# Kernel tuning notes

Measured on AMD Instinct MI355X. Metric: run time of the kernel, lower is better.

## Reference

```python
import jax, jax.numpy as jnp
import numpy as np

INPUT_SIZE = 784
HIDDEN = 512
NUM_CLASSES = 10
BATCH = 65536


def _linear_params(key, fan_in, fan_out):
    # torch nn.Linear default init: U(-1/sqrt(fan_in), 1/sqrt(fan_in))
    kw, kb = jax.random.split(key)
    bound = 1.0 / np.sqrt(fan_in)
    W = jax.random.uniform(kw, (fan_in, fan_out), jnp.float32, -bound, bound)
    b = jax.random.uniform(kb, (fan_out,), jnp.float32, -bound, bound)
    return W, b


def setup_inputs() -> dict:
    key = jax.random.key(0)
    keys = jax.random.split(key, 9)
    inp = {"x": jax.random.normal(keys[0], (BATCH, INPUT_SIZE), jnp.float32)}
    dims = [(INPUT_SIZE, HIDDEN)] + [(HIDDEN, HIDDEN)] * 6 + [(HIDDEN, NUM_CLASSES)]
    for i, (fi, fo) in enumerate(dims):
        W, b = _linear_params(keys[i + 1], fi, fo)
        inp[f"W{i + 1}"] = W
        inp[f"b{i + 1}"] = b
    return inp


def _dropout(x, p, key):
    # torch F.dropout (training=True): inverted dropout, keep prob = 1-p
    keep = jax.random.bernoulli(key, 1.0 - p, x.shape)
    return jnp.where(keep, x / (1.0 - p), 0.0).astype(x.dtype)


def reference(x, W1, b1, W2, b2, W3, b3, W4, b4, W5, b5, W6, b6, W7, b7, W8, b8):
    dk = jax.random.split(jax.random.key(42), 3)
    h = jax.nn.relu(x @ W1 + b1)                       # h1 + relu
    h = jax.nn.relu(_dropout(h @ W2 + b2, 0.2, dk[0])) # h2 + dropout(0.2) + relu
    h = jax.nn.relu(h @ W3 + b3)                       # h3 + relu
    h = jax.nn.relu(_dropout(h @ W4 + b4, 0.3, dk[1])) # h4 + dropout(0.3) + relu
    h = jax.nn.relu(h @ W5 + b5)                       # h5 + relu
    h = jax.nn.relu(_dropout(h @ W6 + b6, 0.5, dk[2])) # h6 + dropout(0.5) + relu
    h = jax.nn.relu(h @ W7 + b7)                       # h7 + relu
    logits = h @ W8 + b8                               # h8
    return jax.nn.softmax(logits, axis=-1)
```

## Files before the change

kernel.cpp:

```cpp
#include <hip/hip_runtime.h>
#include <cstdint>

#define ROTL32(v,n) (((v) << (n)) | ((v) >> (32 - (n))))

__host__ __forceinline__ void tf2x32(uint32_t k0, uint32_t k1,
                                     uint32_t x0, uint32_t x1,
                                     uint32_t& o0, uint32_t& o1)
{
  uint32_t k2 = k0 ^ k1 ^ 0x1BD11BDAu;
  x0 += k0; x1 += k1;
#define TF_RND(r) { x0 += x1; x1 = ROTL32(x1, (r)); x1 ^= x0; }
  TF_RND(13) TF_RND(15) TF_RND(26) TF_RND(6)
  x0 += k1; x1 += k2 + 1u;
  TF_RND(17) TF_RND(29) TF_RND(16) TF_RND(24)
  x0 += k2; x1 += k0 + 2u;
  TF_RND(13) TF_RND(15) TF_RND(26) TF_RND(6)
  x0 += k0; x1 += k1 + 3u;
  TF_RND(17) TF_RND(29) TF_RND(16) TF_RND(24)
  x0 += k1; x1 += k2 + 4u;
  TF_RND(13) TF_RND(15) TF_RND(26) TF_RND(6)
  x0 += k2; x1 += k0 + 5u;
#undef TF_RND
  o0 = x0; o1 = x1;
}

__device__ __forceinline__ void tf2x32_d(uint32_t k0, uint32_t k1,
                                         uint32_t x0, uint32_t x1,
                                         uint32_t& o0, uint32_t& o1)
{
  uint32_t k2 = k0 ^ k1 ^ 0x1BD11BDAu;
  x0 += k0; x1 += k1;
#define R_(r) { x0 += x1; x1 = __builtin_rotateleft32(x1, (r)); x1 ^= x0; }
  R_(13) R_(15) R_(26) R_(6)
  x0 += k1; x1 += k2 + 1u;
  R_(17) R_(29) R_(16) R_(24)
  x0 += k2; x1 += k0 + 2u;
  R_(13) R_(15) R_(26) R_(6)
  x0 += k0; x1 += k1 + 3u;
  R_(17) R_(29) R_(16) R_(24)
  x0 += k1; x1 += k2 + 4u;
  R_(13) R_(15) R_(26) R_(6)
  x0 += k2; x1 += k0 + 5u;
#undef R_
  o0 = x0; o1 = x1;
}

typedef __attribute__((ext_vector_type(8))) _Float16 h16x8;
typedef __attribute__((ext_vector_type(4))) float fl32x4;
typedef __attribute__((ext_vector_type(2))) unsigned long long u64x2;

__device__ __forceinline__ float u2unit_f(uint32_t b) {
  uint32_t r = (b >> 9) | 0x3F800000u;
  float f; __builtin_memcpy(&f, &r, 4); return f - 1.0f;
}

#define GLD16(gp, lp) \
  __builtin_amdgcn_global_load_lds( \
      (__attribute__((address_space(1))) void*)(gp), \
      (__attribute__((address_space(3))) void*)(lp), 16, 0, 0)

#define VMW(n) asm volatile("s_waitcnt vmcnt(" #n ")" ::: "memory")
#define LKW0() asm volatile("s_waitcnt lgkmcnt(0)" ::: "memory")
#define SBAR() asm volatile("s_barrier" ::: "memory")

__global__ __launch_bounds__(256) void cvt_x_f(const float* __restrict__ x,
                                               _Float16* __restrict__ xp,
                                               unsigned long long* __restrict__ m0,
                                               uint32_t k0, uint32_t k1)
{
  int idx = blockIdx.x * 256 + threadIdx.x;
  int row = idx / 104, c = idx - row * 104;
  h16x8 o = {0,0,0,0,0,0,0,0};
  if (c < 98) {
    const fl32x4* p = (const fl32x4*)&x[row * 784 + c * 8];
    fl32x4 a = p[0], b = p[1];
    o[0] = (_Float16)a[0]; o[1] = (_Float16)a[1]; o[2] = (_Float16)a[2]; o[3] = (_Float16)a[3];
    o[4] = (_Float16)b[0]; o[5] = (_Float16)b[1]; o[6] = (_Float16)b[2]; o[7] = (_Float16)b[3];
  }
  *(h16x8*)&xp[row * 832 + c * 8] = o;

  uint32_t lane = threadIdx.x & 63u;
  uint32_t gw = (uint32_t)blockIdx.x * 4u + ((uint32_t)threadIdx.x >> 6);
#pragma unroll
  for (int i = 0; i < 3; ++i) {
    uint32_t wix = gw * 3u + (uint32_t)i;
    uint32_t b1, b2;
    tf2x32_d(k0, k1, 0u, wix * 64u + lane, b1, b2);
    unsigned long long mw = __ballot(u2unit_f(b1 ^ b2) < 0.8f);
    if (lane == 0) m0[wix] = mw;
  }
}

__global__ __launch_bounds__(256) void cvt_w_f(
    const float* __restrict__ W1, const float* __restrict__ W2, const float* __restrict__ W3,
    const float* __restrict__ W4, const float* __restrict__ W5, const float* __restrict__ W6,
    const float* __restrict__ W7, _Float16* __restrict__ WT1, _Float16* __restrict__ WT,
    unsigned long long* __restrict__ m0, uint32_t k0, uint32_t k1)
{
  int b = blockIdx.x;
  if (b < 1666) {
    int idx = b * 256 + threadIdx.x;
    int n = idx / 832, k = idx - n * 832;
    WT1[idx] = (k < 784) ? (_Float16)W1[k * 512 + n] : (_Float16)0.f;
  } else {
    int l = (b - 1666) >> 10;
    int idx = ((b - 1666) & 1023) * 256 + threadIdx.x;
    int n = idx >> 9, k = idx & 511;
    const float* Wp = (l == 0) ? W2 : (l == 1) ? W3 : (l == 2) ? W4
                    : (l == 3) ? W5 : (l == 4) ? W6 : W7;
    WT[l * 262144 + idx] = (_Float16)Wp[k * 512 + n];
  }
  uint32_t lane = threadIdx.x & 63u;
  uint32_t gw = (uint32_t)blockIdx.x * 4u + ((uint32_t)threadIdx.x >> 6);
#pragma unroll
  for (int i = 0; i < 7; ++i) {
    uint32_t wix = 319488u + gw * 7u + (uint32_t)i;
    if (wix < 524288u) {
      uint32_t b1, b2;
      tf2x32_d(k0, k1, 0u, wix * 64u + lane, b1, b2);
      unsigned long long mw = __ballot(u2unit_f(b1 ^ b2) < 0.8f);
      if (lane == 0) m0[wix] = mw;
    }
  }
}

template<bool DROP>
__global__ __launch_bounds__(256, 4) void gemm_r(
    const _Float16* __restrict__ A, const _Float16* __restrict__ BT,
    const float* __restrict__ bias, const unsigned long long* __restrict__ mask,
    float invq, _Float16* __restrict__ C, int K,
    unsigned long long* __restrict__ mout, uint32_t mbase, int tfcap, int tfpp,
    uint32_t mk0, uint32_t mk1, float mq)
{
  __shared__ __align__(16) _Float16 sm[16384];
  const int tid  = threadIdx.x;
  const int lane = tid & 63;
  const int wv   = tid >> 6;
  const int wr   = wv >> 1, wc = wv & 1;
  const int rml  = lane & 15;
  const int kq   = lane >> 4;

  int bid = blockIdx.x;
  int t = (bid & 7) * 256 + (bid >> 3);
  int bm = (t >> 2) * 128;
  int bn = (t & 3) * 128;

  const _Float16* Ab = A + (size_t)bm * K;
  const _Float16* Bb = BT + (size_t)bn * K;

  const int sp   = tid >> 3;
  const int sin  = (tid & 7) ^ (sp & 7);
  const int srow = 2 * sp + (sin >> 2);
  const int sk16 = sin & 3;

  const int rslot = (((rml & 1) << 2) | kq) ^ (rml >> 1);
  const int abase = (wr * 32 + (rml >> 1)) * 64 + rslot * 8;
  const int bbase = 4096 + (wc * 32 + (rml >> 1)) * 64 + rslot * 8;

  fl32x4 acc[4][4];
#pragma unroll
  for (int i = 0; i < 4; ++i)
#pragma unroll
    for (int j = 0; j < 4; ++j)
      acc[i][j] = (fl32x4){0.f, 0.f, 0.f, 0.f};

  const int nst = K >> 5;

#define STAGE(selem, kt) do {                                                  \
    GLD16(Ab + (size_t)srow * K + (kt) * 32 + sk16 * 8,                        \
          sm + (selem) + wv * 512);                                            \
    GLD16(Ab + (size_t)(srow + 64) * K + (kt) * 32 + sk16 * 8,                 \
          sm + (selem) + 2048 + wv * 512);                                     \
    GLD16(Bb + (size_t)srow * K + (kt) * 32 + sk16 * 8,                        \
          sm + (selem) + 4096 + wv * 512);                                     \
    GLD16(Bb + (size_t)(srow + 64) * K + (kt) * 32 + sk16 * 8,                 \
          sm + (selem) + 6144 + wv * 512);                                     \
  } while (0)

  STAGE(0, 0);

  uint64_t mw0 = 0;
  int tfc = 0;
  uint32_t gw = (uint32_t)bid * 4u + (uint32_t)wv;

#pragma unroll 1
  for (int kt = 0; kt < nst; ++kt) {
    const int slot = (kt & 1) * 8192;
    if (kt + 1 < nst) STAGE(8192 - slot, kt + 1);
    if (mout != nullptr) {
      int todo = tfcap - tfc; if (todo > tfpp) todo = tfpp;
      for (int i_ = 0; i_ < todo; ++i_) {
        uint32_t a_, b_;
        tf2x32_d(mk0, mk1, 0u,
                 (mbase + gw * (uint32_t)tfcap + (uint32_t)tfc) * 64u + (uint32_t)lane,
                 a_, b_);
        unsigned long long bal = __ballot(u2unit_f(a_ ^ b_) < mq);
        if (lane == tfc) mw0 = bal;
        ++tfc;
      }
    }
    if (kt + 1 < nst) { VMW(4); } else { VMW(0); }
    SBAR();
    h16x8 af[4], bf[4];
#pragma unroll
    for (int mf = 0; mf < 4; ++mf)
      af[mf] = *(const h16x8*)&sm[slot + abase + mf * 512];
#pragma unroll
    for (int nf = 0; nf < 4; ++nf)
      bf[nf] = *(const h16x8*)&sm[slot + bbase + nf * 512];
#pragma unroll
    for (int mf = 0; mf < 4; ++mf)
#pragma unroll
      for (int nf = 0; nf < 4; ++nf)
        acc[mf][nf] = __builtin_amdgcn_mfma_f32_16x16x32_f16(af[mf], bf[nf], acc[mf][nf], 0, 0, 0);
    SBAR();
  }
#undef STAGE

  if (mout != nullptr && lane < tfcap)
    mout[mbase + gw * (uint32_t)tfcap + (uint32_t)lane] = mw0;

  const int eb = wv * 2176;
  const int lrr = lane >> 1;
  const int cbase = (lane & 1) * 4;

#define EPIHALF(HALF) do {                                                     \
    _Pragma("unroll")                                                          \
    for (int nf = 0; nf < 4; ++nf) {                                           \
      int colq = nf * 16 + rml;                                                \
      float bv = bias[bn + wc * 64 + colq];                                    \
      _Pragma("unroll")                                                        \
      for (int mfh = 0; mfh < 2; ++mfh) {                                      \
        _Pragma("unroll")                                                      \
        for (int r = 0; r < 4; ++r) {                                          \
          int lr = mfh * 16 + kq * 4 + r;                                      \
          float v = fmaxf(acc[(HALF) * 2 + mfh][nf][r] + bv, 0.0f) * invq;     \
          sm[eb + lr * 68 + colq] = (_Float16)v;                               \
        }                                                                      \
      }                                                                        \
    }                                                                          \
    LKW0();                                                                    \
    {                                                                          \
      int grow = bm + wr * 64 + (HALF) * 32 + lrr;                             \
      int col0 = bn + wc * 64;                                                 \
      uint64_t mw = 0;                                                         \
      if (DROP) mw = mask[(size_t)grow * 8 + (size_t)(col0 >> 6)];             \
      _Pragma("unroll")                                                        \
      for (int c = 0; c < 4; ++c) {                                            \
        int cc = cbase + c;                                                    \
        uint64_t lo = *(const uint64_t*)&sm[eb + lrr * 68 + cc * 8];           \
        uint64_t hi = *(const uint64_t*)&sm[eb + lrr * 68 + cc * 8 + 4];       \
        if (DROP) {                                                            \
          uint32_t bits = (uint32_t)(mw >> (cc * 8)) & 0xffu;                  \
          uint64_t klo = 0, khi = 0;                                           \
          if (bits & 0x01u) klo |= 0x000000000000ffffull;                      \
          if (bits & 0x02u) klo |= 0x00000000ffff0000ull;                      \
          if (bits & 0x04u) klo |= 0x0000ffff00000000ull;                      \
          if (bits & 0x08u) klo |= 0xffff000000000000ull;                      \
          if (bits & 0x10u) khi |= 0x000000000000ffffull;                      \
          if (bits & 0x20u) khi |= 0x00000000ffff0000ull;                      \
          if (bits & 0x40u) khi |= 0x0000ffff00000000ull;                      \
          if (bits & 0x80u) khi |= 0xffff000000000000ull;                      \
          lo &= klo; hi &= khi;                                                \
        }                                                                      \
        u64x2 ov; ov[0] = lo; ov[1] = hi;                                      \
        *(u64x2*)&C[(size_t)grow * 512 + col0 + cc * 8] = ov;                  \
      }                                                                        \
    }                                                                          \
  } while (0)

  EPIHALF(0);
  EPIHALF(1);
#undef EPIHALF
}

__global__ __launch_bounds__(256) void head_f(
    const _Float16* __restrict__ H, const float* __restrict__ W8,
    const float* __restrict__ b8, float* __restrict__ out)
{
  __shared__ float Wl[5120];
  for (int i = threadIdx.x; i < 5120; i += 256) Wl[i] = W8[i];
  __syncthreads();
  int lane = threadIdx.x & 63;
  int wv = threadIdx.x >> 6;
  int row = blockIdx.x * 4 + wv;
  h16x8 h = *(const h16x8*)&H[(size_t)row * 512 + lane * 8];
  float acc[10];
#pragma unroll
  for (int n = 0; n < 10; ++n) acc[n] = 0.f;
#pragma unroll
  for (int j = 0; j < 8; ++j) {
    float hf = (float)h[j];
    const float* wrow = &Wl[(lane * 8 + j) * 10];
#pragma unroll
    for (int n = 0; n < 10; ++n) acc[n] += hf * wrow[n];
  }
#pragma unroll
  for (int off = 1; off < 64; off <<= 1) {
#pragma unroll
    for (int n = 0; n < 10; ++n) acc[n] += __shfl_xor(acc[n], off);
  }
  if (lane == 0) {
    float mx = -3.0e38f;
#pragma unroll
    for (int n = 0; n < 10; ++n) { acc[n] += b8[n]; mx = fmaxf(mx, acc[n]); }
    float s = 0.f, e[10];
#pragma unroll
    for (int n = 0; n < 10; ++n) { e[n] = expf(acc[n] - mx); s += e[n]; }
    float is = 1.0f / s;
#pragma unroll
    for (int n = 0; n < 10; ++n) out[(size_t)row * 10 + n] = e[n] * is;
  }
}

extern "C" void kernel_launch(void* const* d_in, const int* in_sizes, int n_in,
                              void* d_out, int out_size, void* d_ws, size_t ws_size,
                              hipStream_t stream) {
  (void)in_sizes; (void)n_in; (void)out_size; (void)ws_size;
  const float* x = (const float*)d_in[0];
  const float* W[8]; const float* B[8];
  for (int i = 0; i < 8; ++i) { W[i] = (const float*)d_in[1 + 2*i]; B[i] = (const float*)d_in[2 + 2*i]; }

  char* w = (char*)d_ws;
  _Float16* xpad = (_Float16*)(w);
  _Float16* hA   = (_Float16*)(w + 109051904);
  _Float16* hB   = (_Float16*)(w + 176160768);
  _Float16* WT1  = (_Float16*)(w + 243269632);
  _Float16* WT   = (_Float16*)(w + 244121600);
  unsigned long long* masks = (unsigned long long*)(w + 247267328);
  unsigned long long* mL0 = masks;
  unsigned long long* mL1 = masks + 524288;
  unsigned long long* mL2 = masks + 1048576;

  uint32_t d00,d01,d10,d11,d20,d21;
  tf2x32(0u, 42u, 0u, 0u, d00, d01);
  tf2x32(0u, 42u, 0u, 1u, d10, d11);
  tf2x32(0u, 42u, 0u, 2u, d20, d21);

  cvt_x_f<<<26624, 256, 0, stream>>>(x, xpad, mL0, d00, d01);
  cvt_w_f<<<7810, 256, 0, stream>>>(W[0],W[1],W[2],W[3],W[4],W[5],W[6], WT1, WT,
                                    mL0, d00, d01);

  dim3 g(2048), b(256);
  gemm_r<false><<<g, b, 0, stream>>>(xpad, WT1,           B[0], nullptr, 1.0f,      hA, 832,
                                     nullptr, 0u, 0, 0, 0u, 0u, 0.f);
  gemm_r<true ><<<g, b, 0, stream>>>(hA,   WT + 0*262144, B[1], mL0,     1.0f/0.8f, hB, 512,
                                     mL1, 0u,       32, 2, d10, d11, 0.7f);
  gemm_r<false><<<g, b, 0, stream>>>(hB,   WT + 1*262144, B[2], nullptr, 1.0f,      hA, 512,
                                     mL1, 262144u,  32, 2, d10, d11, 0.7f);
  gemm_r<true ><<<g, b, 0, stream>>>(hA,   WT + 2*262144, B[3], mL1,     1.0f/0.7f, hB, 512,
                                     mL2, 0u,       32, 2, d20, d21, 0.5f);
  gemm_r<false><<<g, b, 0, stream>>>(hB,   WT + 3*262144, B[4], nullptr, 1.0f,      hA, 512,
                                     mL2, 262144u,  32, 2, d20, d21, 0.5f);
  gemm_r<true ><<<g, b, 0, stream>>>(hA,   WT + 4*262144, B[5], mL2,     2.0f,      hB, 512,
                                     nullptr, 0u, 0, 0, 0u, 0u, 0.f);
  gemm_r<false><<<g, b, 0, stream>>>(hB,   WT + 5*262144, B[6], nullptr, 1.0f,      hA, 512,
                                     nullptr, 0u, 0, 0, 0u, 0u, 0.f);
  head_f<<<16384, 256, 0, stream>>>(hA, W[7], B[7], (float*)d_out);
}
```

Baseline: 676.8 us.

## Fuse final linear head into last GEMM epilogue with partial logits

```diff
diff --git a/kernel.cpp b/kernel.cpp
--- a/kernel.cpp
+++ b/kernel.cpp
@@ -124,13 +124,14 @@
   }
 }
 
-template<bool DROP>
+template<bool DROP, bool HEAD>
 __global__ __launch_bounds__(256, 4) void gemm_r(
     const _Float16* __restrict__ A, const _Float16* __restrict__ BT,
     const float* __restrict__ bias, const unsigned long long* __restrict__ mask,
     float invq, _Float16* __restrict__ C, int K,
     unsigned long long* __restrict__ mout, uint32_t mbase, int tfcap, int tfpp,
-    uint32_t mk0, uint32_t mk1, float mq)
+    uint32_t mk0, uint32_t mk1, float mq,
+    const float* __restrict__ W8g, float* __restrict__ plog)
 {
   __shared__ __align__(16) _Float16 sm[16384];
   const int tid  = threadIdx.x;
@@ -219,6 +220,45 @@
 
   if (mout != nullptr && lane < tfcap)
     mout[mbase + gw * (uint32_t)tfcap + (uint32_t)lane] = mw0;
+
+  if (HEAD) {
+    __syncthreads();
+    float* W8l = (float*)sm;
+    for (int i = tid; i < 1280; i += 256) {
+      int k = i / 10, c = i - k * 10;
+      W8l[i] = W8g[(size_t)(bn + k) * 10 + c];
+    }
+    __syncthreads();
+    float* pout = plog + (size_t)((t & 3) * 2 + wc) * 655360;
+#pragma unroll
+    for (int mf = 0; mf < 4; ++mf) {
+#pragma unroll
+      for (int r = 0; r < 4; ++r) {
+        float p[10];
+#pragma unroll
+        for (int c = 0; c < 10; ++c) p[c] = 0.f;
+#pragma unroll
+        for (int nf = 0; nf < 4; ++nf) {
+          int kc = wc * 64 + nf * 16 + rml;
+          float v = fmaxf(acc[mf][nf][r] + bias[bn + kc], 0.0f);
+          const float* wrow = &W8l[kc * 10];
+#pragma unroll
+          for (int c = 0; c < 10; ++c) p[c] += v * wrow[c];
+        }
+#pragma unroll
+        for (int off = 1; off < 16; off <<= 1) {
+#pragma unroll
+          for (int c = 0; c < 10; ++c) p[c] += __shfl_xor(p[c], off);
+        }
+        if (rml == 0) {
+          int row = bm + wr * 64 + mf * 16 + kq * 4 + r;
+#pragma unroll
+          for (int c = 0; c < 10; ++c) pout[(size_t)row * 10 + c] = p[c];
+        }
+      }
+    }
+    return;
+  }
 
   const int eb = wv * 2176;
   const int lrr = lane >> 1;
@@ -274,43 +314,29 @@
 #undef EPIHALF
 }
 
-__global__ __launch_bounds__(256) void head_f(
-    const _Float16* __restrict__ H, const float* __restrict__ W8,
-    const float* __restrict__ b8, float* __restrict__ out)
-{
-  __shared__ float Wl[5120];
-  for (int i = threadIdx.x; i < 5120; i += 256) Wl[i] = W8[i];
-  __syncthreads();
-  int lane = threadIdx.x & 63;
-  int wv = threadIdx.x >> 6;
-  int row = blockIdx.x * 4 + wv;
-  h16x8 h = *(const h16x8*)&H[(size_t)row * 512 + lane * 8];
-  float acc[10];
-#pragma unroll
-  for (int n = 0; n < 10; ++n) acc[n] = 0.f;
-#pragma unroll
-  for (int j = 0; j < 8; ++j) {
-    float hf = (float)h[j];
-    const float* wrow = &Wl[(lane * 8 + j) * 10];
-#pragma unroll
-    for (int n = 0; n < 10; ++n) acc[n] += hf * wrow[n];
-  }
-#pragma unroll
-  for (int off = 1; off < 64; off <<= 1) {
-#pragma unroll
-    for (int n = 0; n < 10; ++n) acc[n] += __shfl_xor(acc[n], off);
-  }
-  if (lane == 0) {
-    float mx = -3.0e38f;
-#pragma unroll
-    for (int n = 0; n < 10; ++n) { acc[n] += b8[n]; mx = fmaxf(mx, acc[n]); }
-    float s = 0.f, e[10];
-#pragma unroll
-    for (int n = 0; n < 10; ++n) { e[n] = expf(acc[n] - mx); s += e[n]; }
-    float is = 1.0f / s;
-#pragma unroll
-    for (int n = 0; n < 10; ++n) out[(size_t)row * 10 + n] = e[n] * is;
-  }
+__global__ __launch_bounds__(256) void smax_k(const float* __restrict__ plog,
+                                              const float* __restrict__ b8,
+                                              float* __restrict__ out)
+{
+  int row = blockIdx.x * 256 + threadIdx.x;
+  float l[10];
+#pragma unroll
+  for (int c = 0; c < 10; ++c) l[c] = b8[c];
+#pragma unroll
+  for (int s = 0; s < 8; ++s) {
+    const float* pr = &plog[(size_t)s * 655360 + (size_t)row * 10];
+#pragma unroll
+    for (int c = 0; c < 10; ++c) l[c] += pr[c];
+  }
+  float mx = l[0];
+#pragma unroll
+  for (int c = 1; c < 10; ++c) mx = fmaxf(mx, l[c]);
+  float sum = 0.f, e[10];
+#pragma unroll
+  for (int c = 0; c < 10; ++c) { e[c] = expf(l[c] - mx); sum += e[c]; }
+  float is = 1.0f / sum;
+#pragma unroll
+  for (int c = 0; c < 10; ++c) out[(size_t)row * 10 + c] = e[c] * is;
 }
 
 extern "C" void kernel_launch(void* const* d_in, const int* in_sizes, int n_in,
@@ -323,6 +349,7 @@
 
   char* w = (char*)d_ws;
   _Float16* xpad = (_Float16*)(w);
+  float*    plog = (float*)(w);
   _Float16* hA   = (_Float16*)(w + 109051904);
   _Float16* hB   = (_Float16*)(w + 176160768);
   _Float16* WT1  = (_Float16*)(w + 243269632);
@@ -342,19 +369,19 @@
                                     mL0, d00, d01);
 
   dim3 g(2048), b(256);
-  gemm_r<false><<<g, b, 0, stream>>>(xpad, WT1,           B[0], nullptr, 1.0f,      hA, 832,
-                                     nullptr, 0u, 0, 0, 0u, 0u, 0.f);
-  gemm_r<true ><<<g, b, 0, stream>>>(hA,   WT + 0*262144, B[1], mL0,     1.0f/0.8f, hB, 512,
-                                     mL1, 0u,       32, 2, d10, d11, 0.7f);
-  gemm_r<false><<<g, b, 0, stream>>>(hB,   WT + 1*262144, B[2], nullptr, 1.0f,      hA, 512,
-                                     mL1, 262144u,  32, 2, d10, d11, 0.7f);
-  gemm_r<true ><<<g, b, 0, stream>>>(hA,   WT + 2*262144, B[3], mL1,     1.0f/0.7f, hB, 512,
-                                     mL2, 0u,       32, 2, d20, d21, 0.5f);
-  gemm_r<false><<<g, b, 0, stream>>>(hB,   WT + 3*262144, B[4], nullptr, 1.0f,      hA, 512,
-                                     mL2, 262144u,  32, 2, d20, d21, 0.5f);
-  gemm_r<true ><<<g, b, 0, stream>>>(hA,   WT + 4*262144, B[5], mL2,     2.0f,      hB, 512,
-                                     nullptr, 0u, 0, 0, 0u, 0u, 0.f);
-  gemm_r<false><<<g, b, 0, stream>>>(hB,   WT + 5*262144, B[6], nullptr, 1.0f,      hA, 512,
-                                     nullptr, 0u, 0, 0, 0u, 0u, 0.f);
-  head_f<<<16384, 256, 0, stream>>>(hA, W[7], B[7], (float*)d_out);
-}
+  gemm_r<false,false><<<g, b, 0, stream>>>(xpad, WT1,           B[0], nullptr, 1.0f,      hA, 832,
+                                     nullptr, 0u, 0, 0, 0u, 0u, 0.f, nullptr, nullptr);
+  gemm_r<true ,false><<<g, b, 0, stream>>>(hA,   WT + 0*262144, B[1], mL0,     1.0f/0.8f, hB, 512,
+                                     mL1, 0u,       32, 2, d10, d11, 0.7f, nullptr, nullptr);
+  gemm_r<false,false><<<g, b, 0, stream>>>(hB,   WT + 1*262144, B[2], nullptr, 1.0f,      hA, 512,
+                                     mL1, 262144u,  32, 2, d10, d11, 0.7f, nullptr, nullptr);
+  gemm_r<true ,false><<<g, b, 0, stream>>>(hA,   WT + 2*262144, B[3], mL1,     1.0f/0.7f, hB, 512,
+                                     mL2, 0u,       32, 2, d20, d21, 0.5f, nullptr, nullptr);
+  gemm_r<false,false><<<g, b, 0, stream>>>(hB,   WT + 3*262144, B[4], nullptr, 1.0f,      hA, 512,
+                                     mL2, 262144u,  32, 2, d20, d21, 0.5f, nullptr, nullptr);
+  gemm_r<true ,false><<<g, b, 0, stream>>>(hA,   WT + 4*262144, B[5], mL2,     2.0f,      hB, 512,
+                                     nullptr, 0u, 0, 0, 0u, 0u, 0.f, nullptr, nullptr);
+  gemm_r<false,true ><<<g, b, 0, stream>>>(hB,   WT + 5*262144, B[6], nullptr, 1.0f,      hA, 512,
+                                     nullptr, 0u, 0, 0, 0u, 0u, 0.f, W[7], plog);
+  smax_k<<<256, 256, 0, stream>>>(plog, B[7], (float*)d_out);
+}
```

Result: faster. 654.0 us (-3.4%).
